# Kernel tuning notes

Measured on AMD Instinct MI355X. Metric: run time of the kernel, lower is better.

## Reference

```python
import jax, jax.numpy as jnp
import numpy as np

B, S, D, MAX_LEN = 4, 2048, 512, 2048
V = 2 * MAX_LEN + 1  # embedding table size
POS_MAX = 3000


def setup_inputs() -> dict:
    key = jax.random.key(0)
    k1, k2, k3 = jax.random.split(key, 3)
    x = jax.random.normal(k1, (B, S, D), dtype=jnp.float32)
    emb_table = jax.random.normal(k2, (V, D), dtype=jnp.float32) * 0.02
    positions = jnp.sort(jax.random.randint(k3, (B, S), 0, POS_MAX), axis=-1)
    return {"x": x, "emb_table": emb_table, "positions": positions}


def reference(x, emb_table, positions):
    # x: [B,S,D], emb_table: [2M+1, D], positions: [B,S] int
    Bc, Sc, _ = x.shape
    Vc = emb_table.shape[0]
    M = (Vc - 1) // 2
    # rel[b,i,j] = clamp(pos_i - pos_j, -M, M) + M   -> index into table
    rel = jnp.clip(positions[:, :, None] - positions[:, None, :], -M, M) + M  # [B,S,S]
    # mean_j emb[rel[b,i,j]] == (occurrence counts over V) @ table / S
    # counts[b,i,v] = #{j : rel[b,i,j] == v}; identical math, no [B,S,S,D] tensor.
    b_idx = jnp.arange(Bc)[:, None, None]
    i_idx = jnp.arange(Sc)[None, :, None]
    counts = jnp.zeros((Bc, Sc, Vc), dtype=x.dtype).at[b_idx, i_idx, rel].add(1.0)
    mean_emb = jnp.einsum('bsv,vd->bsd', counts, emb_table) / Sc  # [B,S,D]
    return x + mean_emb
```

## Files before the change

kernel.cpp:

```cpp
#include <hip/hip_runtime.h>
#include <hip/hip_bf16.h>
#include <cstdint>

#define NB 4
#define NS 2048
#define ND 512
#define NM 2048
#define NV 4097
#define NP 3000
#define TROW 8192
#define CCC 5104
#define EVW 4128
#define RSW 3080

typedef __bf16 bf16x8 __attribute__((ext_vector_type(8)));
typedef float f32x4 __attribute__((ext_vector_type(4)));

typedef const unsigned int __attribute__((address_space(1)))* as1_u32p;
typedef unsigned int __attribute__((address_space(3)))* as3_u32p;

__device__ __forceinline__ void gll16(const void* g, void* l) {
  __builtin_amdgcn_global_load_lds((as1_u32p)g, (as3_u32p)l, 16, 0, 0);
}

__device__ __forceinline__ unsigned short f2bf(float f) {
  union { __bf16 b; unsigned short u; } cv;
  cv.b = (__bf16)f;
  return cv.u;
}

__device__ __forceinline__ int lbound_dev(const int* a, int n, int key) {
  int lo = 0, hi = n;
  while (lo < hi) { int mid = (lo + hi) >> 1; if (a[mid] < key) lo = mid + 1; else hi = mid; }
  return lo;
}

__global__ void k1_hist(const int* __restrict__ pos, unsigned int* __restrict__ hist) {
  __shared__ unsigned int h[NP];
  int b = blockIdx.x, tid = threadIdx.x;
  for (int i = tid; i < NP; i += 256) h[i] = 0u;
  __syncthreads();
  const int* pb = pos + b * NS;
  for (int i = tid; i < NS; i += 256) atomicAdd(&h[pb[i]], 1u);
  __syncthreads();
  unsigned int* hb = hist + b * NP;
  for (int i = tid; i < NP; i += 256) hb[i] = h[i];
}

__global__ void k1b_rs(const int* __restrict__ pos, int* __restrict__ rs) {
  int t = blockIdx.x * 256 + threadIdx.x;
  int b = blockIdx.y;
  if (t > 3072) return;
  rs[b * RSW + t] = lbound_dev(pos + b * NS, NS, t);
}

__global__ void k2_htrev(const unsigned int* __restrict__ hist, unsigned short* __restrict__ HT) {
  int idx = blockIdx.x * 256 + threadIdx.x;
  int b = idx >> 14, rem = idx & 16383;
  int u = rem >> 10, t8 = rem & 1023;
  const unsigned int* hb = hist + b * NP;
  int basep = CCC + u - t8 * 8;
  union { unsigned short us[8]; uint4 v4; } pk;
#pragma unroll
  for (int e = 0; e < 8; ++e) {
    int p = basep - e;
    float f = (p >= 0 && p < NP) ? (float)hb[p] : 0.0f;
    pk.us[e] = f2bf(f);
  }
  *(uint4*)(HT + (size_t)(b * 16 + u) * TROW + t8 * 8) = pk.v4;
}

__global__ void k3_ebf(const float* __restrict__ emb, unsigned short* __restrict__ EB) {
  __shared__ float tile[64][65];
  int v0 = blockIdx.x * 64, d0 = blockIdx.y * 64, tid = threadIdx.x;
  int c = tid & 63, r0 = tid >> 6;
#pragma unroll
  for (int k = 0; k < 16; ++k) {
    int r = k * 4 + r0;
    int v = v0 + r;
    float val = 0.f;
    if (v < NV && v != 0 && v != (NV - 1)) val = emb[(size_t)v * ND + d0 + c];
    tile[r][c] = val;
  }
  __syncthreads();
  int vv0 = (tid & 7) * 8;
#pragma unroll
  for (int k2 = 0; k2 < 2; ++k2) {
    int dd = (tid >> 3) + k2 * 32;
    if (v0 + vv0 + 8 <= EVW) {
      union { unsigned short us[8]; uint4 v4; } pk;
#pragma unroll
      for (int e = 0; e < 8; ++e) pk.us[e] = f2bf(tile[vv0 + e][dd]);
      *(uint4*)(EB + (size_t)(d0 + dd) * EVW + v0 + vv0) = pk.v4;
    }
  }
}

__global__ __launch_bounds__(256, 4)
void k4_gemm(const unsigned short* __restrict__ HT, const unsigned short* __restrict__ EB,
             const int* __restrict__ rs, const float* __restrict__ x,
             const float* __restrict__ emb, float* __restrict__ out) {
  int Q0 = blockIdx.x * 64, d0 = blockIdx.y * 128, b = blockIdx.z;
  int tid = threadIdx.x, w = tid >> 6, lane = tid & 63;
  int wm = w >> 1, wn = w & 1;
  __shared__ unsigned short As[3][2048];
  __shared__ unsigned short Bs[3][4096];

  const unsigned short* HTb = HT + (size_t)b * 16 * TROW;
  int ul = lane & 15, gl = lane >> 4;

  int v_lo = (Q0 > 951) ? ((Q0 - 951) & ~31) : 0;
  int v_hi = Q0 + 2112; if (v_hi > EVW) v_hi = EVW;
  int nt = (v_hi - v_lo) >> 5;

  f32x4 acc[2][4];
#pragma unroll
  for (int a1 = 0; a1 < 2; ++a1)
#pragma unroll
    for (int a2 = 0; a2 < 4; ++a2) { f32x4 z = {0.f, 0.f, 0.f, 0.f}; acc[a1][a2] = z; }

  const unsigned short* asrc_lane = HTb + ul * TROW + gl * 8;

  auto stage = [&](int sbuf, int t) {
    int kk = v_lo + t * 32;
    int t0 = CCC - Q0 - NM - 16 * w + kk;
    gll16(asrc_lane + t0, &As[sbuf][w * 512]);
#pragma unroll
    for (int ci = 0; ci < 2; ++ci) {
      int c = w + ci * 4;
      const unsigned short* bsrc = EB + (size_t)(d0 + c * 16 + ul) * EVW + kk + gl * 8;
      gll16(bsrc, &Bs[sbuf][c * 512]);
    }
  };

  stage(0, 0);
  stage(1, 1);

  int aoff = (lane >> 4) * 128 + (lane & 15) * 8;
  int s0 = 0, s1 = 1, s2 = 2;
  for (int t = 0; t < nt; ++t) {
    if (t + 1 < nt) asm volatile("s_waitcnt vmcnt(3) lgkmcnt(0)" ::: "memory");
    else            asm volatile("s_waitcnt vmcnt(0) lgkmcnt(0)" ::: "memory");
    __builtin_amdgcn_s_barrier();
    if (t + 2 < nt) stage(s2, t + 2);

    bf16x8 af[2], bfr[4];
#pragma unroll
    for (int mf = 0; mf < 2; ++mf)
      af[mf] = *reinterpret_cast<const bf16x8*>(&As[s0][(wm * 2 + mf) * 512 + aoff]);
#pragma unroll
    for (int nf = 0; nf < 4; ++nf)
      bfr[nf] = *reinterpret_cast<const bf16x8*>(&Bs[s0][(wn * 4 + nf) * 512 + aoff]);
    __builtin_amdgcn_s_setprio(1);
#pragma unroll
    for (int mf = 0; mf < 2; ++mf)
#pragma unroll
      for (int nf = 0; nf < 4; ++nf)
        acc[mf][nf] = __builtin_amdgcn_mfma_f32_16x16x32_bf16(af[mf], bfr[nf], acc[mf][nf], 0, 0, 0);
    __builtin_amdgcn_s_setprio(0);
    int tmp = s0; s0 = s1; s1 = s2; s2 = tmp;
  }

  const int* rsb = rs + b * RSW;
  const float* xb = x + (size_t)b * NS * ND;
  float* outb = out + (size_t)b * NS * ND;
  int col = lane & 15, rb4 = (lane >> 4) * 4;
#pragma unroll
  for (int nf = 0; nf < 4; ++nf) {
    int dcol = d0 + wn * 64 + nf * 16 + col;
    float e0v = emb[dcol];
    float eMv = emb[(size_t)(NV - 1) * ND + dcol];
#pragma unroll
    for (int mf = 0; mf < 2; ++mf) {
#pragma unroll
      for (int j = 0; j < 4; ++j) {
        int q = Q0 + wm * 32 + mf * 16 + rb4 + j;
        if (q >= NP) continue;
        int i0 = rsb[q], i1 = rsb[q + 1];
        if (i0 == i1) continue;
        int cge = (q >= NM) ? rsb[q - NM + 1] : 0;
        int cle = (q + NM < NP) ? (NS - rsb[q + NM]) : 0;
        float val = (acc[mf][nf][j] + (float)cge * eMv + (float)cle * e0v) * (1.0f / (float)NS);
        for (int i = i0; i < i1; ++i)
          outb[(size_t)i * ND + dcol] = xb[(size_t)i * ND + dcol] + val;
      }
    }
  }
}

extern "C" void kernel_launch(void* const* d_in, const int* in_sizes, int n_in,
                              void* d_out, int out_size, void* d_ws, size_t ws_size,
                              hipStream_t stream) {
  const float* x = (const float*)d_in[0];
  const float* emb = (const float*)d_in[1];
  const int* pos = (const int*)d_in[2];
  float* out = (float*)d_out;

  char* ws = (char*)d_ws;
  unsigned short* HT = (unsigned short*)(ws);
  unsigned short* EB = (unsigned short*)(ws + 1048576);
  unsigned int* hist = (unsigned int*)(ws + 5275648);
  int* rs = (int*)(ws + 5323648);

  hipLaunchKernelGGL(k1_hist, dim3(NB), dim3(256), 0, stream, pos, hist);
  hipLaunchKernelGGL(k1b_rs, dim3(13, NB), dim3(256), 0, stream, pos, rs);
  hipLaunchKernelGGL(k2_htrev, dim3(256), dim3(256), 0, stream, hist, HT);
  hipLaunchKernelGGL(k3_ebf, dim3(65, 8), dim3(256), 0, stream, emb, EB);
  hipLaunchKernelGGL(k4_gemm, dim3(47, 4, NB), dim3(256), 0, stream, HT, EB, rs, x, emb, out);
}
```

Baseline: 178.7 us.

## Merge prep kernels into one launch and enlarge GEMM M-tile to 96

Folds the three preprocessing kernels (row-start search, reversed histogram to bf16, embedding transpose to bf16) into a single launch that dispatches on block index, removing two launch gaps. The GEMM tile grows from 64 to 96 query rows per block, with three M fragments per wave and extra A-staging loads done by two of the waves, adjusted wait counts, and launch bounds lowered to 2 blocks per CU. This raises B-tile reuse and cuts the grid from 752 to 512 blocks, at the cost of more registers and LDS per block, lower occupancy and a longer K range per block.

```diff
diff --git a/kernel.cpp b/kernel.cpp
--- a/kernel.cpp
+++ b/kernel.cpp
@@ -47,75 +47,80 @@
   for (int i = tid; i < NP; i += 256) hb[i] = h[i];
 }
 
-__global__ void k1b_rs(const int* __restrict__ pos, int* __restrict__ rs) {
-  int t = blockIdx.x * 256 + threadIdx.x;
-  int b = blockIdx.y;
-  if (t > 3072) return;
-  rs[b * RSW + t] = lbound_dev(pos + b * NS, NS, t);
-}
-
-__global__ void k2_htrev(const unsigned int* __restrict__ hist, unsigned short* __restrict__ HT) {
-  int idx = blockIdx.x * 256 + threadIdx.x;
-  int b = idx >> 14, rem = idx & 16383;
-  int u = rem >> 10, t8 = rem & 1023;
-  const unsigned int* hb = hist + b * NP;
-  int basep = CCC + u - t8 * 8;
-  union { unsigned short us[8]; uint4 v4; } pk;
-#pragma unroll
-  for (int e = 0; e < 8; ++e) {
-    int p = basep - e;
-    float f = (p >= 0 && p < NP) ? (float)hb[p] : 0.0f;
-    pk.us[e] = f2bf(f);
-  }
-  *(uint4*)(HT + (size_t)(b * 16 + u) * TROW + t8 * 8) = pk.v4;
-}
-
-__global__ void k3_ebf(const float* __restrict__ emb, unsigned short* __restrict__ EB) {
+__global__ void k23_prep(const int* __restrict__ pos, const unsigned int* __restrict__ hist,
+                         const float* __restrict__ emb, unsigned short* __restrict__ HT,
+                         unsigned short* __restrict__ EB, int* __restrict__ rs) {
   __shared__ float tile[64][65];
-  int v0 = blockIdx.x * 64, d0 = blockIdx.y * 64, tid = threadIdx.x;
-  int c = tid & 63, r0 = tid >> 6;
-#pragma unroll
-  for (int k = 0; k < 16; ++k) {
-    int r = k * 4 + r0;
-    int v = v0 + r;
-    float val = 0.f;
-    if (v < NV && v != 0 && v != (NV - 1)) val = emb[(size_t)v * ND + d0 + c];
-    tile[r][c] = val;
-  }
-  __syncthreads();
-  int vv0 = (tid & 7) * 8;
-#pragma unroll
-  for (int k2 = 0; k2 < 2; ++k2) {
-    int dd = (tid >> 3) + k2 * 32;
-    if (v0 + vv0 + 8 <= EVW) {
-      union { unsigned short us[8]; uint4 v4; } pk;
-#pragma unroll
-      for (int e = 0; e < 8; ++e) pk.us[e] = f2bf(tile[vv0 + e][dd]);
-      *(uint4*)(EB + (size_t)(d0 + dd) * EVW + v0 + vv0) = pk.v4;
-    }
-  }
-}
-
-__global__ __launch_bounds__(256, 4)
+  int blk = blockIdx.x, tid = threadIdx.x;
+  if (blk < 52) {
+    int b = blk & 3, chunk = blk >> 2;
+    int t = chunk * 256 + tid;
+    if (t <= 3072) rs[b * RSW + t] = lbound_dev(pos + b * NS, NS, t);
+    return;
+  }
+  if (blk < 308) {
+    int idx = (blk - 52) * 256 + tid;
+    int b = idx >> 14, rem = idx & 16383;
+    int u = rem >> 10, t8 = rem & 1023;
+    const unsigned int* hb = hist + b * NP;
+    int basep = CCC + u - t8 * 8;
+    union { unsigned short us[8]; uint4 v4; } pk;
+#pragma unroll
+    for (int e = 0; e < 8; ++e) {
+      int p = basep - e;
+      float f = (p >= 0 && p < NP) ? (float)hb[p] : 0.0f;
+      pk.us[e] = f2bf(f);
+    }
+    *(uint4*)(HT + (size_t)(b * 16 + u) * TROW + t8 * 8) = pk.v4;
+    return;
+  }
+  {
+    int blk3 = blk - 308;
+    int v0 = (blk3 % 65) * 64, d0 = (blk3 / 65) * 64;
+    int c = tid & 63, r0 = tid >> 6;
+#pragma unroll
+    for (int k = 0; k < 16; ++k) {
+      int r = k * 4 + r0;
+      int v = v0 + r;
+      float val = 0.f;
+      if (v < NV && v != 0 && v != (NV - 1)) val = emb[(size_t)v * ND + d0 + c];
+      tile[r][c] = val;
+    }
+    __syncthreads();
+    int vv0 = (tid & 7) * 8;
+#pragma unroll
+    for (int k2 = 0; k2 < 2; ++k2) {
+      int dd = (tid >> 3) + k2 * 32;
+      if (v0 + vv0 + 8 <= EVW) {
+        union { unsigned short us[8]; uint4 v4; } pk;
+#pragma unroll
+        for (int e = 0; e < 8; ++e) pk.us[e] = f2bf(tile[vv0 + e][dd]);
+        *(uint4*)(EB + (size_t)(d0 + dd) * EVW + v0 + vv0) = pk.v4;
+      }
+    }
+  }
+}
+
+__global__ __launch_bounds__(256, 2)
 void k4_gemm(const unsigned short* __restrict__ HT, const unsigned short* __restrict__ EB,
              const int* __restrict__ rs, const float* __restrict__ x,
              const float* __restrict__ emb, float* __restrict__ out) {
-  int Q0 = blockIdx.x * 64, d0 = blockIdx.y * 128, b = blockIdx.z;
+  int Q0 = blockIdx.x * 96, d0 = blockIdx.y * 128, b = blockIdx.z;
   int tid = threadIdx.x, w = tid >> 6, lane = tid & 63;
   int wm = w >> 1, wn = w & 1;
-  __shared__ unsigned short As[3][2048];
+  __shared__ unsigned short As[3][3072];
   __shared__ unsigned short Bs[3][4096];
 
   const unsigned short* HTb = HT + (size_t)b * 16 * TROW;
   int ul = lane & 15, gl = lane >> 4;
 
   int v_lo = (Q0 > 951) ? ((Q0 - 951) & ~31) : 0;
-  int v_hi = Q0 + 2112; if (v_hi > EVW) v_hi = EVW;
+  int v_hi = Q0 + 2144; if (v_hi > EVW) v_hi = EVW;
   int nt = (v_hi - v_lo) >> 5;
 
-  f32x4 acc[2][4];
-#pragma unroll
-  for (int a1 = 0; a1 < 2; ++a1)
+  f32x4 acc[3][4];
+#pragma unroll
+  for (int a1 = 0; a1 < 3; ++a1)
 #pragma unroll
     for (int a2 = 0; a2 < 4; ++a2) { f32x4 z = {0.f, 0.f, 0.f, 0.f}; acc[a1][a2] = z; }
 
@@ -123,8 +128,11 @@
 
   auto stage = [&](int sbuf, int t) {
     int kk = v_lo + t * 32;
-    int t0 = CCC - Q0 - NM - 16 * w + kk;
-    gll16(asrc_lane + t0, &As[sbuf][w * 512]);
+    gll16(asrc_lane + (CCC - Q0 - NM - 16 * w + kk), &As[sbuf][w * 512]);
+    if (w < 2) {
+      int c = 4 + w;
+      gll16(asrc_lane + (CCC - Q0 - NM - 16 * c + kk), &As[sbuf][c * 512]);
+    }
 #pragma unroll
     for (int ci = 0; ci < 2; ++ci) {
       int c = w + ci * 4;
@@ -139,21 +147,25 @@
   int aoff = (lane >> 4) * 128 + (lane & 15) * 8;
   int s0 = 0, s1 = 1, s2 = 2;
   for (int t = 0; t < nt; ++t) {
-    if (t + 1 < nt) asm volatile("s_waitcnt vmcnt(3) lgkmcnt(0)" ::: "memory");
-    else            asm volatile("s_waitcnt vmcnt(0) lgkmcnt(0)" ::: "memory");
+    if (t + 1 < nt) {
+      if (w < 2) asm volatile("s_waitcnt vmcnt(4) lgkmcnt(0)" ::: "memory");
+      else       asm volatile("s_waitcnt vmcnt(3) lgkmcnt(0)" ::: "memory");
+    } else {
+      asm volatile("s_waitcnt vmcnt(0) lgkmcnt(0)" ::: "memory");
+    }
     __builtin_amdgcn_s_barrier();
     if (t + 2 < nt) stage(s2, t + 2);
 
-    bf16x8 af[2], bfr[4];
-#pragma unroll
-    for (int mf = 0; mf < 2; ++mf)
-      af[mf] = *reinterpret_cast<const bf16x8*>(&As[s0][(wm * 2 + mf) * 512 + aoff]);
+    bf16x8 af[3], bfr[4];
+#pragma unroll
+    for (int mf = 0; mf < 3; ++mf)
+      af[mf] = *reinterpret_cast<const bf16x8*>(&As[s0][(wm * 3 + mf) * 512 + aoff]);
 #pragma unroll
     for (int nf = 0; nf < 4; ++nf)
       bfr[nf] = *reinterpret_cast<const bf16x8*>(&Bs[s0][(wn * 4 + nf) * 512 + aoff]);
     __builtin_amdgcn_s_setprio(1);
 #pragma unroll
-    for (int mf = 0; mf < 2; ++mf)
+    for (int mf = 0; mf < 3; ++mf)
 #pragma unroll
       for (int nf = 0; nf < 4; ++nf)
         acc[mf][nf] = __builtin_amdgcn_mfma_f32_16x16x32_bf16(af[mf], bfr[nf], acc[mf][nf], 0, 0, 0);
@@ -171,10 +183,10 @@
     float e0v = emb[dcol];
     float eMv = emb[(size_t)(NV - 1) * ND + dcol];
 #pragma unroll
-    for (int mf = 0; mf < 2; ++mf) {
+    for (int mf = 0; mf < 3; ++mf) {
 #pragma unroll
       for (int j = 0; j < 4; ++j) {
-        int q = Q0 + wm * 32 + mf * 16 + rb4 + j;
+        int q = Q0 + wm * 48 + mf * 16 + rb4 + j;
         if (q >= NP) continue;
         int i0 = rsb[q], i1 = rsb[q + 1];
         if (i0 == i1) continue;
@@ -203,8 +215,6 @@
   int* rs = (int*)(ws + 5323648);
 
   hipLaunchKernelGGL(k1_hist, dim3(NB), dim3(256), 0, stream, pos, hist);
-  hipLaunchKernelGGL(k1b_rs, dim3(13, NB), dim3(256), 0, stream, pos, rs);
-  hipLaunchKernelGGL(k2_htrev, dim3(256), dim3(256), 0, stream, hist, HT);
-  hipLaunchKernelGGL(k3_ebf, dim3(65, 8), dim3(256), 0, stream, emb, EB);
-  hipLaunchKernelGGL(k4_gemm, dim3(47, 4, NB), dim3(256), 0, stream, HT, EB, rs, x, emb, out);
-}
+  hipLaunchKernelGGL(k23_prep, dim3(828), dim3(256), 0, stream, pos, hist, emb, HT, EB, rs);
+  hipLaunchKernelGGL(k4_gemm, dim3(32, 4, NB), dim3(256), 0, stream, HT, EB, rs, x, emb, out);
+}
```

Result: slower. 187.0 us (+4.7%).
